# Optimization experiments

Hardware: AMD Instinct MI355X
Metric: run time of the kernel (lower is better)

## Reference

```python
import jax, jax.numpy as jnp
import numpy as np

B, S, C, P, M, H = 64, 512, 862, 96, 512, 128  # batch, seq_len, enc_in, pred_len, mem_num, hid_size


def setup_inputs() -> dict:
    key = jax.random.key(0)
    ks = jax.random.split(key, 8)
    x = jax.random.normal(ks[0], (B, S, C), dtype=jnp.float32)
    # nn.Linear default init scale ~ 1/sqrt(fan_in)
    W1 = jax.random.normal(ks[1], (H, S), dtype=jnp.float32) / np.float32(np.sqrt(S))
    b1 = jnp.zeros((H,), dtype=jnp.float32)
    Wp = jax.random.normal(ks[2], (H, H), dtype=jnp.float32) / np.float32(np.sqrt(H))
    bp = jnp.zeros((H,), dtype=jnp.float32)
    W2 = jax.random.normal(ks[3], (P, 2 * H), dtype=jnp.float32) / np.float32(np.sqrt(2 * H))
    b2 = jnp.zeros((P,), dtype=jnp.float32)
    # xavier_normal_ with relu gain: std = sqrt(2) * sqrt(2/(fan_in+fan_out))
    mem_std = np.float32(np.sqrt(2.0) * np.sqrt(2.0 / (M + H)))
    memory = jax.random.normal(ks[4], (M, H), dtype=jnp.float32) * mem_std
    return dict(x=x, W1=W1, b1=b1, Wp=Wp, bp=bp, W2=W2, b2=b2, memory=memory)


def reference(x, W1, b1, Wp, bp, W2, b2, memory):
    b, s, c = x.shape
    # get_repre: Linear1 over seq dim, sigmoid, projector
    r = jax.nn.sigmoid(jnp.einsum('bsc,hs->bch', x, W1) + b1)   # [B, C, H]
    r = jnp.einsum('bch,gh->bcg', r, Wp) + bp                    # [B, C, H]
    r = r.reshape(-1, H)                                         # [N, H], N = B*C
    # memory_enhance: codebook attention (topk/distance loss does not affect output)
    att = jax.nn.softmax(jnp.einsum('nd,fd->nf', r, memory), axis=1)  # [N, M]
    out = jnp.einsum('nf,fd->nd', att, memory)                        # [N, H]
    rep = jnp.concatenate([out, r], axis=1).reshape(b, c, 2 * H)      # [B, C, 2H]
    # predict: Linear2 then permute to [B, pred_len, C]
    res = jnp.einsum('bcd,pd->bcp', rep, W2) + b2
    return jnp.transpose(res, (0, 2, 1))
```

## Files before the change

kernel.cpp:

```cpp
#include <hip/hip_runtime.h>
#include <hip/hip_bf16.h>

typedef __attribute__((ext_vector_type(4))) float f32x4;
typedef __attribute__((ext_vector_type(8))) short s16x8;

#define DEVI __device__ __forceinline__

constexpr int S = 512, C = 862, P = 96, H = 128, BATCH = 64;

DEVI short f2bf(float f) {
  unsigned u = __builtin_bit_cast(unsigned, f);
  u += 0x7fffu + ((u >> 16) & 1u);
  return (short)(u >> 16);
}

DEVI unsigned pk2(float a, float b) {
  return (unsigned)(unsigned short)f2bf(a) | ((unsigned)(unsigned short)f2bf(b) << 16);
}

DEVI s16x8 mk8(const float* v) {
  s16x8 r;
#pragma unroll
  for (int i = 0; i < 8; ++i) r[i] = f2bf(v[i]);
  return r;
}

DEVI void gload16(const void* g, void* l) {
  __builtin_amdgcn_global_load_lds(
      (const __attribute__((address_space(1))) void*)g,
      (__attribute__((address_space(3))) void*)l, 16, 0, 0);
}

template <int NK>
DEVI void redistN(const unsigned* p01, const unsigned* p23, int sA, int hi,
                  s16x8* f) {
#pragma unroll
  for (int kc = 0; kc < NK; ++kc) {
    unsigned a0 = __shfl(p01[2 * kc], sA),      b0 = __shfl(p01[2 * kc + 1], sA);
    unsigned a1 = __shfl(p23[2 * kc], sA),      b1 = __shfl(p23[2 * kc + 1], sA);
    unsigned a2 = __shfl(p01[2 * kc], sA + 16), b2 = __shfl(p01[2 * kc + 1], sA + 16);
    unsigned a3 = __shfl(p23[2 * kc], sA + 16), b3 = __shfl(p23[2 * kc + 1], sA + 16);
    union { s16x8 v; unsigned u[4]; } t;
    t.u[0] = hi ? b0 : a0;
    t.u[1] = hi ? b1 : a1;
    t.u[2] = hi ? b2 : a2;
    t.u[3] = hi ? b3 : a3;
    f[kc] = t.v;
  }
}

__global__ __launch_bounds__(256) void k0_convert(
    const float* __restrict__ W1, const float* __restrict__ Wp,
    const float* __restrict__ W2, const float* __restrict__ mem,
    short* __restrict__ W1b, short* __restrict__ WpS, short* __restrict__ W2b,
    short* __restrict__ membS, short* __restrict__ memTS) {
  int i = blockIdx.x * 256 + threadIdx.x;
  if (i < 65536) { W1b[i] = f2bf(W1[i]); return; }
  i -= 65536;
  if (i < 16384) {
    int g = i >> 7, h = i & 127;
    WpS[(g << 7) + (h ^ ((g & 7) << 3))] = f2bf(Wp[i]);
    return;
  }
  i -= 16384;
  if (i < 24576) { W2b[i] = f2bf(W2[i]); return; }
  i -= 24576;
  if (i < 65536) {
    int f = i >> 7, d = i & 127;
    short v = f2bf(mem[i]);
    membS[((f >> 6) << 13) + ((f & 63) << 7) + (d ^ ((f & 7) << 3))] = v;
    memTS[((f >> 6) << 13) + (d << 6) + ((f & 63) ^ ((d & 7) << 3))] = v;
  }
}

__global__ __launch_bounds__(512, 2) void k12_fused(
    const float* __restrict__ x, const short* __restrict__ W1b,
    const float* __restrict__ b1, const short* __restrict__ WpS,
    const float* __restrict__ bp, const short* __restrict__ membS,
    const short* __restrict__ memTS, const short* __restrict__ W2b,
    const float* __restrict__ b2, float* __restrict__ out) {
  __shared__ __align__(16) char lds[65536];
  short* xt0 = (short*)(lds);
  short* xt1 = (short*)(lds + 16384);
  short* w1t0 = (short*)(lds + 32768);
  short* w1t1 = (short*)(lds + 49152);
  float* resf = (float*)lds;

  const int b = blockIdx.y, c0 = blockIdx.x * 128;
  const int valid = (C - c0 < 128) ? (C - c0) : 128;
  const int tid = threadIdx.x, l = tid & 63, w = tid >> 6;
  const int l15 = l & 15, l4 = l >> 4;
  const int sA = l15 + 32 * (l4 & 1);
  const int hi = (l4 >> 1) & 1;
  const int xr = (l15 & 7) << 4;
  const int cb = l4 * 16;
  const int rloc = 16 * w + l15;

  s16x8 rb[4];
  {
    const int cme = tid & 127, o2 = tid >> 7;
    const bool cv = (c0 + cme) < C;
    const float* xsrc0 = x + (size_t)b * S * C + c0 + cme;
    const int hh = tid >> 2, qq = tid & 3;

    f32x4 acc[8];
#pragma unroll
    for (int t = 0; t < 8; ++t) acc[t] = (f32x4){0.f, 0.f, 0.f, 0.f};

    float xv[2][8];
    s16x8 wv[2];
    {
#pragma unroll
      for (int j = 0; j < 2; ++j) {
        const float* src = xsrc0 + (size_t)((o2 + j * 4) * 8) * C;
#pragma unroll
        for (int i = 0; i < 8; ++i) xv[j][i] = cv ? src[(size_t)i * C] : 0.f;
      }
      const short* wsrc = W1b + hh * 512;
      wv[0] = *(const s16x8*)&wsrc[qq * 8];
      wv[1] = *(const s16x8*)&wsrc[(qq + 4) * 8];
    }

    for (int kt = 0; kt < 8; ++kt) {
      short* xt = (kt & 1) ? xt1 : xt0;
      short* w1t = (kt & 1) ? w1t1 : w1t0;
#pragma unroll
      for (int j = 0; j < 2; ++j)
        *(s16x8*)&xt[cme * 64 + ((o2 + j * 4) ^ (cme & 7)) * 8] = mk8(xv[j]);
      *(s16x8*)&w1t[hh * 64 + (qq ^ (hh & 7)) * 8] = wv[0];
      *(s16x8*)&w1t[hh * 64 + ((qq + 4) ^ (hh & 7)) * 8] = wv[1];
      __syncthreads();
      if (kt < 7) {
        int kn = kt + 1;
#pragma unroll
        for (int j = 0; j < 2; ++j) {
          const float* src = xsrc0 + (size_t)(kn * 64 + (o2 + j * 4) * 8) * C;
#pragma unroll
          for (int i = 0; i < 8; ++i) xv[j][i] = cv ? src[(size_t)i * C] : 0.f;
        }
        const short* wsrc = W1b + hh * 512 + kn * 64;
        wv[0] = *(const s16x8*)&wsrc[qq * 8];
        wv[1] = *(const s16x8*)&wsrc[(qq + 4) * 8];
      }
      s16x8 bx[2];
#pragma unroll
      for (int kc = 0; kc < 2; ++kc)
        bx[kc] = *(const s16x8*)&xt[rloc * 64 + ((kc * 4 + l4) ^ (l15 & 7)) * 8];
#pragma unroll
      for (int t = 0; t < 8; ++t) {
#pragma unroll
        for (int kc = 0; kc < 2; ++kc) {
          s16x8 af = *(const s16x8*)&w1t[(t * 16 + l15) * 64 + ((kc * 4 + l4) ^ (l15 & 7)) * 8];
          acc[t] = __builtin_amdgcn_mfma_f32_16x16x32_bf16(af, bx[kc], acc[t], 0, 0, 0);
        }
      }
      if (kt == 7) __syncthreads();
    }

    unsigned p01[8], p23[8];
#pragma unroll
    for (int t = 0; t < 8; ++t) {
      f32x4 bq = *(const f32x4*)&b1[t * 16 + l4 * 4];
      float s0 = 1.f / (1.f + __expf(-(acc[t][0] + bq[0])));
      float s1 = 1.f / (1.f + __expf(-(acc[t][1] + bq[1])));
      float s2 = 1.f / (1.f + __expf(-(acc[t][2] + bq[2])));
      float s3 = 1.f / (1.f + __expf(-(acc[t][3] + bq[3])));
      p01[t] = pk2(s0, s1);
      p23[t] = pk2(s2, s3);
    }
    redistN<4>(p01, p23, sA, hi, rb);
  }

  {
    const char* gwp = (const char*)WpS;
    const char* gmb = (const char*)membS;
    const char* gmt = (const char*)memTS;
#pragma unroll
    for (int i = 0; i < 4; ++i) {
      int o = (w * 4 + i) * 1024;
      gload16(gwp + o + l * 16, lds + 32768 + o);
    }
#pragma unroll
    for (int i = 0; i < 2; ++i) {
      int o = (w * 2 + i) * 1024;
      gload16(gmb + o + l * 16, lds + o);
      gload16(gmt + o + l * 16, lds + 16384 + o);
    }
  }
  __syncthreads();

  unsigned rpk01[8], rpk23[8];
  {
    const char* bufWp = lds + 32768;
#pragma unroll
    for (int gt = 0; gt < 8; ++gt) {
      f32x4 acc = (f32x4){0.f, 0.f, 0.f, 0.f};
#pragma unroll
      for (int kc = 0; kc < 4; ++kc) {
        s16x8 af = *(const s16x8*)(bufWp + (gt * 16 + l15) * 256 + ((kc * 64 + cb) ^ xr));
        acc = __builtin_amdgcn_mfma_f32_16x16x32_bf16(af, rb[kc], acc, 0, 0, 0);
      }
      f32x4 bq = *(const f32x4*)&bp[gt * 16 + l4 * 4];
      rpk01[gt] = pk2(acc[0] + bq[0], acc[1] + bq[1]);
      rpk23[gt] = pk2(acc[2] + bq[2], acc[3] + bq[3]);
    }
  }
  s16x8 r2f[4];
  redistN<4>(rpk01, rpk23, sA, hi, r2f);
  __syncthreads();

  float m_run = -1e30f, s_run = 0.f;
  f32x4 oacc[8];
#pragma unroll
  for (int dt = 0; dt < 8; ++dt) oacc[dt] = (f32x4){0.f, 0.f, 0.f, 0.f};

  for (int s = 0; s < 8; ++s) {
    char* bufp = lds + ((s & 1) << 15);
    if (s < 7) {
      char* bufn = lds + (((s + 1) & 1) << 15);
      const char* gmb = (const char*)membS + (size_t)(s + 1) * 16384;
      const char* gmt = (const char*)memTS + (size_t)(s + 1) * 16384;
#pragma unroll
      for (int i = 0; i < 2; ++i) {
        int o = (w * 2 + i) * 1024;
        gload16(gmb + o + l * 16, bufn + o);
        gload16(gmt + o + l * 16, bufn + 16384 + o);
      }
    }
    f32x4 lg[4];
#pragma unroll
    for (int ft = 0; ft < 4; ++ft) {
      lg[ft] = (f32x4){0.f, 0.f, 0.f, 0.f};
#pragma unroll
      for (int kc = 0; kc < 4; ++kc) {
        s16x8 af = *(const s16x8*)(bufp + (ft * 16 + l15) * 256 + ((kc * 64 + cb) ^ xr));
        lg[ft] = __builtin_amdgcn_mfma_f32_16x16x32_bf16(af, r2f[kc], lg[ft], 0, 0, 0);
      }
    }
    float mx = lg[0][0];
#pragma unroll
    for (int ft = 0; ft < 4; ++ft)
#pragma unroll
      for (int e = 0; e < 4; ++e) mx = fmaxf(mx, lg[ft][e]);
    mx = fmaxf(mx, __shfl_xor(mx, 16));
    mx = fmaxf(mx, __shfl_xor(mx, 32));
    float mn = fmaxf(m_run, mx);
    float sc = __expf(m_run - mn);
    float ps = 0.f;
#pragma unroll
    for (int ft = 0; ft < 4; ++ft)
#pragma unroll
      for (int e = 0; e < 4; ++e) {
        float p = __expf(lg[ft][e] - mn);
        lg[ft][e] = p;
        ps += p;
      }
    ps += __shfl_xor(ps, 16);
    ps += __shfl_xor(ps, 32);
    s_run = s_run * sc + ps;
    m_run = mn;
#pragma unroll
    for (int dt = 0; dt < 8; ++dt)
#pragma unroll
      for (int e = 0; e < 4; ++e) oacc[dt][e] *= sc;
    unsigned ppk01[4], ppk23[4];
#pragma unroll
    for (int ft = 0; ft < 4; ++ft) {
      ppk01[ft] = pk2(lg[ft][0], lg[ft][1]);
      ppk23[ft] = pk2(lg[ft][2], lg[ft][3]);
    }
    s16x8 pf[2];
    redistN<2>(ppk01, ppk23, sA, hi, pf);
#pragma unroll
    for (int dt = 0; dt < 8; ++dt) {
#pragma unroll
      for (int kc = 0; kc < 2; ++kc) {
        s16x8 af = *(const s16x8*)(bufp + 16384 + (dt * 16 + l15) * 128 + ((kc * 64 + cb) ^ xr));
        oacc[dt] = __builtin_amdgcn_mfma_f32_16x16x32_bf16(af, pf[kc], oacc[dt], 0, 0, 0);
      }
    }
    __syncthreads();
  }

  s16x8 of[4];
  {
    float inv = 1.f / s_run;
    unsigned opk01[8], opk23[8];
#pragma unroll
    for (int dt = 0; dt < 8; ++dt) {
      opk01[dt] = pk2(oacc[dt][0] * inv, oacc[dt][1] * inv);
      opk23[dt] = pk2(oacc[dt][2] * inv, oacc[dt][3] * inv);
    }
    redistN<4>(opk01, opk23, sA, hi, of);
  }

#pragma unroll
  for (int pt = 0; pt < 6; ++pt) {
    f32x4 acc = (f32x4){0.f, 0.f, 0.f, 0.f};
#pragma unroll
    for (int kc = 0; kc < 4; ++kc) {
      s16x8 af = *(const s16x8*)&W2b[(pt * 16 + l15) * 256 + kc * 32 + l4 * 8];
      acc = __builtin_amdgcn_mfma_f32_16x16x32_bf16(af, of[kc], acc, 0, 0, 0);
    }
#pragma unroll
    for (int kc = 0; kc < 4; ++kc) {
      s16x8 af = *(const s16x8*)&W2b[(pt * 16 + l15) * 256 + 128 + kc * 32 + l4 * 8];
      acc = __builtin_amdgcn_mfma_f32_16x16x32_bf16(af, r2f[kc], acc, 0, 0, 0);
    }
    f32x4 bq = *(const f32x4*)&b2[pt * 16 + l4 * 4];
#pragma unroll
    for (int e = 0; e < 4; ++e)
      resf[rloc * 97 + pt * 16 + l4 * 4 + e] = acc[e] + bq[e];
  }
  __syncthreads();
  {
    int c = tid & 127, p0 = tid >> 7;
    if (c < valid) {
      float* dst = out + (size_t)b * P * C + c0 + c;
#pragma unroll
      for (int j = 0; j < 24; ++j) {
        int p = p0 + j * 4;
        dst[(size_t)p * C] = resf[c * 97 + p];
      }
    }
  }
}

extern "C" void kernel_launch(void* const* d_in, const int* in_sizes, int n_in,
                              void* d_out, int out_size, void* d_ws, size_t ws_size,
                              hipStream_t stream) {
  const float* x   = (const float*)d_in[0];
  const float* W1  = (const float*)d_in[1];
  const float* b1  = (const float*)d_in[2];
  const float* Wp  = (const float*)d_in[3];
  const float* bpv = (const float*)d_in[4];
  const float* W2  = (const float*)d_in[5];
  const float* b2  = (const float*)d_in[6];
  const float* mem = (const float*)d_in[7];
  char* ws = (char*)d_ws;
  short* W1b   = (short*)(ws);
  short* WpS   = (short*)(ws + 131072);
  short* W2b   = (short*)(ws + 163840);
  short* membS = (short*)(ws + 212992);
  short* memTS = (short*)(ws + 344064);
  float* outp = (float*)d_out;

  k0_convert<<<672, 256, 0, stream>>>(W1, Wp, W2, mem, W1b, WpS, W2b, membS, memTS);
  dim3 grid(7, BATCH);
  k12_fused<<<grid, 512, 0, stream>>>(x, W1b, b1, WpS, bpv, membS, memTS, W2b, b2, outp);
}
```

Measured before the change: 83.85 us.

## Software-pipeline codebook attention loop and skip online-softmax rescale when max is stable

Restructures the memory-attention loop so the score MFMAs for chunk i+1 run alongside the value MFMAs for chunk i, with separate double buffers for the memory and transposed-memory tiles. It also adds a lazy-rescale test that skips rescaling the running max and accumulator unless the new max exceeds the old by more than 8, and raises launch bounds from 2 to 4 blocks per SM. This aims to hide softmax latency and LDS load stalls and to cut ALU work. The risks are extra register pressure from the 4-block bound, which may cause spills, and a loss of precision if probabilities grow as large as e^8.

```diff
diff --git a/kernel.cpp b/kernel.cpp
--- a/kernel.cpp
+++ b/kernel.cpp
@@ -73,7 +73,7 @@
   }
 }
 
-__global__ __launch_bounds__(512, 2) void k12_fused(
+__global__ __launch_bounds__(512, 4) void k12_fused(
     const float* __restrict__ x, const short* __restrict__ W1b,
     const float* __restrict__ b1, const short* __restrict__ WpS,
     const float* __restrict__ bp, const short* __restrict__ membS,
@@ -174,7 +174,6 @@
   {
     const char* gwp = (const char*)WpS;
     const char* gmb = (const char*)membS;
-    const char* gmt = (const char*)memTS;
 #pragma unroll
     for (int i = 0; i < 4; ++i) {
       int o = (w * 4 + i) * 1024;
@@ -184,7 +183,6 @@
     for (int i = 0; i < 2; ++i) {
       int o = (w * 2 + i) * 1024;
       gload16(gmb + o + l * 16, lds + o);
-      gload16(gmt + o + l * 16, lds + 16384 + o);
     }
   }
   __syncthreads();
@@ -207,33 +205,21 @@
   }
   s16x8 r2f[4];
   redistN<4>(rpk01, rpk23, sA, hi, r2f);
-  __syncthreads();
-
-  float m_run = -1e30f, s_run = 0.f;
+
+  float m_run, s_run;
   f32x4 oacc[8];
 #pragma unroll
   for (int dt = 0; dt < 8; ++dt) oacc[dt] = (f32x4){0.f, 0.f, 0.f, 0.f};
-
-  for (int s = 0; s < 8; ++s) {
-    char* bufp = lds + ((s & 1) << 15);
-    if (s < 7) {
-      char* bufn = lds + (((s + 1) & 1) << 15);
-      const char* gmb = (const char*)membS + (size_t)(s + 1) * 16384;
-      const char* gmt = (const char*)memTS + (size_t)(s + 1) * 16384;
-#pragma unroll
-      for (int i = 0; i < 2; ++i) {
-        int o = (w * 2 + i) * 1024;
-        gload16(gmb + o + l * 16, bufn + o);
-        gload16(gmt + o + l * 16, bufn + 16384 + o);
-      }
-    }
+  s16x8 pfb[2][2];
+
+  {
     f32x4 lg[4];
 #pragma unroll
     for (int ft = 0; ft < 4; ++ft) {
       lg[ft] = (f32x4){0.f, 0.f, 0.f, 0.f};
 #pragma unroll
       for (int kc = 0; kc < 4; ++kc) {
-        s16x8 af = *(const s16x8*)(bufp + (ft * 16 + l15) * 256 + ((kc * 64 + cb) ^ xr));
+        s16x8 af = *(const s16x8*)(lds + (ft * 16 + l15) * 256 + ((kc * 64 + cb) ^ xr));
         lg[ft] = __builtin_amdgcn_mfma_f32_16x16x32_bf16(af, r2f[kc], lg[ft], 0, 0, 0);
       }
     }
@@ -244,43 +230,130 @@
       for (int e = 0; e < 4; ++e) mx = fmaxf(mx, lg[ft][e]);
     mx = fmaxf(mx, __shfl_xor(mx, 16));
     mx = fmaxf(mx, __shfl_xor(mx, 32));
-    float mn = fmaxf(m_run, mx);
-    float sc = __expf(m_run - mn);
+    m_run = mx;
     float ps = 0.f;
-#pragma unroll
-    for (int ft = 0; ft < 4; ++ft)
+    unsigned ppk01[4], ppk23[4];
+#pragma unroll
+    for (int ft = 0; ft < 4; ++ft) {
 #pragma unroll
       for (int e = 0; e < 4; ++e) {
-        float p = __expf(lg[ft][e] - mn);
+        float p = __expf(lg[ft][e] - m_run);
         lg[ft][e] = p;
         ps += p;
       }
+      ppk01[ft] = pk2(lg[ft][0], lg[ft][1]);
+      ppk23[ft] = pk2(lg[ft][2], lg[ft][3]);
+    }
     ps += __shfl_xor(ps, 16);
     ps += __shfl_xor(ps, 32);
-    s_run = s_run * sc + ps;
-    m_run = mn;
-#pragma unroll
-    for (int dt = 0; dt < 8; ++dt)
-#pragma unroll
-      for (int e = 0; e < 4; ++e) oacc[dt][e] *= sc;
-    unsigned ppk01[4], ppk23[4];
-#pragma unroll
-    for (int ft = 0; ft < 4; ++ft) {
-      ppk01[ft] = pk2(lg[ft][0], lg[ft][1]);
-      ppk23[ft] = pk2(lg[ft][2], lg[ft][3]);
-    }
-    s16x8 pf[2];
-    redistN<2>(ppk01, ppk23, sA, hi, pf);
+    s_run = ps;
+    redistN<2>(ppk01, ppk23, sA, hi, pfb[0]);
+  }
+  __syncthreads();
+  {
+    const char* gmb = (const char*)membS + 16384;
+    const char* gmt = (const char*)memTS;
+#pragma unroll
+    for (int i = 0; i < 2; ++i) {
+      int o = (w * 2 + i) * 1024;
+      gload16(gmb + o + l * 16, lds + 16384 + o);
+      gload16(gmt + o + l * 16, lds + 32768 + o);
+    }
+  }
+
+#pragma unroll
+  for (int i = 0; i < 7; ++i) {
+    __syncthreads();
+    if (i < 6) {
+      const char* gmb = (const char*)membS + (size_t)(i + 2) * 16384;
+#pragma unroll
+      for (int j2 = 0; j2 < 2; ++j2) {
+        int o = (w * 2 + j2) * 1024;
+        gload16(gmb + o + l * 16, lds + ((i & 1) << 14) + o);
+      }
+    }
+    {
+      const char* gmt = (const char*)memTS + (size_t)(i + 1) * 16384;
+#pragma unroll
+      for (int j2 = 0; j2 < 2; ++j2) {
+        int o = (w * 2 + j2) * 1024;
+        gload16(gmt + o + l * 16, lds + 32768 + (((i + 1) & 1) << 14) + o);
+      }
+    }
+    f32x4 lg[4];
+    {
+      const char* bmb = lds + (((i + 1) & 1) << 14);
+#pragma unroll
+      for (int ft = 0; ft < 4; ++ft) {
+        lg[ft] = (f32x4){0.f, 0.f, 0.f, 0.f};
+#pragma unroll
+        for (int kc = 0; kc < 4; ++kc) {
+          s16x8 af = *(const s16x8*)(bmb + (ft * 16 + l15) * 256 + ((kc * 64 + cb) ^ xr));
+          lg[ft] = __builtin_amdgcn_mfma_f32_16x16x32_bf16(af, r2f[kc], lg[ft], 0, 0, 0);
+        }
+      }
+    }
+    {
+      const char* bmt = lds + 32768 + ((i & 1) << 14);
+#pragma unroll
+      for (int dt = 0; dt < 8; ++dt) {
+#pragma unroll
+        for (int kc = 0; kc < 2; ++kc) {
+          s16x8 af = *(const s16x8*)(bmt + (dt * 16 + l15) * 128 + ((kc * 64 + cb) ^ xr));
+          oacc[dt] = __builtin_amdgcn_mfma_f32_16x16x32_bf16(af, pfb[i & 1][kc], oacc[dt], 0, 0, 0);
+        }
+      }
+    }
+    {
+      float mx = lg[0][0];
+#pragma unroll
+      for (int ft = 0; ft < 4; ++ft)
+#pragma unroll
+        for (int e = 0; e < 4; ++e) mx = fmaxf(mx, lg[ft][e]);
+      mx = fmaxf(mx, __shfl_xor(mx, 16));
+      mx = fmaxf(mx, __shfl_xor(mx, 32));
+      if (!__all(mx <= m_run + 8.f)) {
+        float mn = fmaxf(m_run, mx);
+        float sc = __expf(m_run - mn);
+        s_run *= sc;
+        m_run = mn;
+#pragma unroll
+        for (int dt = 0; dt < 8; ++dt)
+#pragma unroll
+          for (int e = 0; e < 4; ++e) oacc[dt][e] *= sc;
+      }
+      float ps = 0.f;
+      unsigned ppk01[4], ppk23[4];
+#pragma unroll
+      for (int ft = 0; ft < 4; ++ft) {
+#pragma unroll
+        for (int e = 0; e < 4; ++e) {
+          float p = __expf(lg[ft][e] - m_run);
+          lg[ft][e] = p;
+          ps += p;
+        }
+        ppk01[ft] = pk2(lg[ft][0], lg[ft][1]);
+        ppk23[ft] = pk2(lg[ft][2], lg[ft][3]);
+      }
+      ps += __shfl_xor(ps, 16);
+      ps += __shfl_xor(ps, 32);
+      s_run += ps;
+      redistN<2>(ppk01, ppk23, sA, hi, pfb[(i + 1) & 1]);
+    }
+  }
+  __syncthreads();
+  {
+    const char* bmt = lds + 32768 + 16384;
 #pragma unroll
     for (int dt = 0; dt < 8; ++dt) {
 #pragma unroll
       for (int kc = 0; kc < 2; ++kc) {
-        s16x8 af = *(const s16x8*)(bufp + 16384 + (dt * 16 + l15) * 128 + ((kc * 64 + cb) ^ xr));
-        oacc[dt] = __builtin_amdgcn_mfma_f32_16x16x32_bf16(af, pf[kc], oacc[dt], 0, 0, 0);
-      }
-    }
-    __syncthreads();
-  }
+        s16x8 af = *(const s16x8*)(bmt + (dt * 16 + l15) * 128 + ((kc * 64 + cb) ^ xr));
+        oacc[dt] = __builtin_amdgcn_mfma_f32_16x16x32_bf16(af, pfb[1][kc], oacc[dt], 0, 0, 0);
+      }
+    }
+  }
+  __syncthreads();
 
   s16x8 of[4];
   {
```

Result: no change. 83.41 us (-0.5%).

## Shrink LDS footprint, restage memory buffers, and skip softmax rescale when max stable

Applied to the files above, without the earlier changes.

Cuts shared memory from 64KB to about 48.5KB by single-buffering the W1/x tiles and loading the transposed memory tile each step without prefetch. Only the memory (logit) tile stays double-buffered. Launch bounds are raised from 2 to 6 blocks per CU to allow more concurrent blocks. The online softmax now skips rescaling the accumulators unless the new max exceeds the running max by more than 8, which saves exp and multiply work. The costs are more barriers per step and a non-prefetched transposed-memory load, and the lazy rescale allows exponentials up to e^8 before rescaling.

```diff
diff --git a/kernel.cpp b/kernel.cpp
--- a/kernel.cpp
+++ b/kernel.cpp
@@ -73,17 +73,13 @@
   }
 }
 
-__global__ __launch_bounds__(512, 2) void k12_fused(
+__global__ __launch_bounds__(512, 6) void k12_fused(
     const float* __restrict__ x, const short* __restrict__ W1b,
     const float* __restrict__ b1, const short* __restrict__ WpS,
     const float* __restrict__ bp, const short* __restrict__ membS,
     const short* __restrict__ memTS, const short* __restrict__ W2b,
     const float* __restrict__ b2, float* __restrict__ out) {
-  __shared__ __align__(16) char lds[65536];
-  short* xt0 = (short*)(lds);
-  short* xt1 = (short*)(lds + 16384);
-  short* w1t0 = (short*)(lds + 32768);
-  short* w1t1 = (short*)(lds + 49152);
+  __shared__ __align__(16) char lds[49664];
   float* resf = (float*)lds;
 
   const int b = blockIdx.y, c0 = blockIdx.x * 128;
@@ -98,6 +94,8 @@
 
   s16x8 rb[4];
   {
+    short* xt = (short*)lds;
+    short* w1t = (short*)(lds + 16384);
     const int cme = tid & 127, o2 = tid >> 7;
     const bool cv = (c0 + cme) < C;
     const float* xsrc0 = x + (size_t)b * S * C + c0 + cme;
@@ -122,8 +120,6 @@
     }
 
     for (int kt = 0; kt < 8; ++kt) {
-      short* xt = (kt & 1) ? xt1 : xt0;
-      short* w1t = (kt & 1) ? w1t1 : w1t0;
 #pragma unroll
       for (int j = 0; j < 2; ++j)
         *(s16x8*)&xt[cme * 64 + ((o2 + j * 4) ^ (cme & 7)) * 8] = mk8(xv[j]);
@@ -154,7 +150,22 @@
           acc[t] = __builtin_amdgcn_mfma_f32_16x16x32_bf16(af, bx[kc], acc[t], 0, 0, 0);
         }
       }
-      if (kt == 7) __syncthreads();
+      __syncthreads();
+    }
+
+    {
+      const char* gwp = (const char*)WpS;
+      const char* gmb = (const char*)membS;
+#pragma unroll
+      for (int i = 0; i < 4; ++i) {
+        int o = (w * 4 + i) * 1024;
+        gload16(gwp + o + l * 16, lds + 16384 + o);
+      }
+#pragma unroll
+      for (int i = 0; i < 2; ++i) {
+        int o = (w * 2 + i) * 1024;
+        gload16(gmb + o + l * 16, lds + o);
+      }
     }
 
     unsigned p01[8], p23[8];
@@ -170,28 +181,11 @@
     }
     redistN<4>(p01, p23, sA, hi, rb);
   }
-
-  {
-    const char* gwp = (const char*)WpS;
-    const char* gmb = (const char*)membS;
-    const char* gmt = (const char*)memTS;
-#pragma unroll
-    for (int i = 0; i < 4; ++i) {
-      int o = (w * 4 + i) * 1024;
-      gload16(gwp + o + l * 16, lds + 32768 + o);
-    }
-#pragma unroll
-    for (int i = 0; i < 2; ++i) {
-      int o = (w * 2 + i) * 1024;
-      gload16(gmb + o + l * 16, lds + o);
-      gload16(gmt + o + l * 16, lds + 16384 + o);
-    }
-  }
   __syncthreads();
 
   unsigned rpk01[8], rpk23[8];
   {
-    const char* bufWp = lds + 32768;
+    const char* bufWp = lds + 16384;
 #pragma unroll
     for (int gt = 0; gt < 8; ++gt) {
       f32x4 acc = (f32x4){0.f, 0.f, 0.f, 0.f};
@@ -207,80 +201,96 @@
   }
   s16x8 r2f[4];
   redistN<4>(rpk01, rpk23, sA, hi, r2f);
-  __syncthreads();
 
   float m_run = -1e30f, s_run = 0.f;
   f32x4 oacc[8];
 #pragma unroll
   for (int dt = 0; dt < 8; ++dt) oacc[dt] = (f32x4){0.f, 0.f, 0.f, 0.f};
 
-  for (int s = 0; s < 8; ++s) {
-    char* bufp = lds + ((s & 1) << 15);
-    if (s < 7) {
-      char* bufn = lds + (((s + 1) & 1) << 15);
-      const char* gmb = (const char*)membS + (size_t)(s + 1) * 16384;
-      const char* gmt = (const char*)memTS + (size_t)(s + 1) * 16384;
+  for (int s5 = 0; s5 < 8; ++s5) {
+    __syncthreads();
+    {
+      const char* gmt = (const char*)memTS + (size_t)s5 * 16384;
 #pragma unroll
       for (int i = 0; i < 2; ++i) {
         int o = (w * 2 + i) * 1024;
-        gload16(gmb + o + l * 16, bufn + o);
-        gload16(gmt + o + l * 16, bufn + 16384 + o);
+        gload16(gmt + o + l * 16, lds + 32768 + o);
+      }
+    }
+    if (s5 < 7) {
+      const char* gmb = (const char*)membS + (size_t)(s5 + 1) * 16384;
+#pragma unroll
+      for (int i = 0; i < 2; ++i) {
+        int o = (w * 2 + i) * 1024;
+        gload16(gmb + o + l * 16, lds + (((s5 + 1) & 1) << 14) + o);
       }
     }
     f32x4 lg[4];
-#pragma unroll
-    for (int ft = 0; ft < 4; ++ft) {
-      lg[ft] = (f32x4){0.f, 0.f, 0.f, 0.f};
-#pragma unroll
-      for (int kc = 0; kc < 4; ++kc) {
-        s16x8 af = *(const s16x8*)(bufp + (ft * 16 + l15) * 256 + ((kc * 64 + cb) ^ xr));
-        lg[ft] = __builtin_amdgcn_mfma_f32_16x16x32_bf16(af, r2f[kc], lg[ft], 0, 0, 0);
-      }
-    }
-    float mx = lg[0][0];
-#pragma unroll
-    for (int ft = 0; ft < 4; ++ft)
-#pragma unroll
-      for (int e = 0; e < 4; ++e) mx = fmaxf(mx, lg[ft][e]);
-    mx = fmaxf(mx, __shfl_xor(mx, 16));
-    mx = fmaxf(mx, __shfl_xor(mx, 32));
-    float mn = fmaxf(m_run, mx);
-    float sc = __expf(m_run - mn);
-    float ps = 0.f;
-#pragma unroll
-    for (int ft = 0; ft < 4; ++ft)
-#pragma unroll
-      for (int e = 0; e < 4; ++e) {
-        float p = __expf(lg[ft][e] - mn);
-        lg[ft][e] = p;
-        ps += p;
-      }
-    ps += __shfl_xor(ps, 16);
-    ps += __shfl_xor(ps, 32);
-    s_run = s_run * sc + ps;
-    m_run = mn;
-#pragma unroll
-    for (int dt = 0; dt < 8; ++dt)
-#pragma unroll
-      for (int e = 0; e < 4; ++e) oacc[dt][e] *= sc;
-    unsigned ppk01[4], ppk23[4];
-#pragma unroll
-    for (int ft = 0; ft < 4; ++ft) {
-      ppk01[ft] = pk2(lg[ft][0], lg[ft][1]);
-      ppk23[ft] = pk2(lg[ft][2], lg[ft][3]);
+    {
+      const char* bmb = lds + ((s5 & 1) << 14);
+#pragma unroll
+      for (int ft = 0; ft < 4; ++ft) {
+        lg[ft] = (f32x4){0.f, 0.f, 0.f, 0.f};
+#pragma unroll
+        for (int kc = 0; kc < 4; ++kc) {
+          s16x8 af = *(const s16x8*)(bmb + (ft * 16 + l15) * 256 + ((kc * 64 + cb) ^ xr));
+          lg[ft] = __builtin_amdgcn_mfma_f32_16x16x32_bf16(af, r2f[kc], lg[ft], 0, 0, 0);
+        }
+      }
     }
     s16x8 pf[2];
-    redistN<2>(ppk01, ppk23, sA, hi, pf);
-#pragma unroll
-    for (int dt = 0; dt < 8; ++dt) {
-#pragma unroll
-      for (int kc = 0; kc < 2; ++kc) {
-        s16x8 af = *(const s16x8*)(bufp + 16384 + (dt * 16 + l15) * 128 + ((kc * 64 + cb) ^ xr));
-        oacc[dt] = __builtin_amdgcn_mfma_f32_16x16x32_bf16(af, pf[kc], oacc[dt], 0, 0, 0);
-      }
+    {
+      float mx = lg[0][0];
+#pragma unroll
+      for (int ft = 0; ft < 4; ++ft)
+#pragma unroll
+        for (int e = 0; e < 4; ++e) mx = fmaxf(mx, lg[ft][e]);
+      mx = fmaxf(mx, __shfl_xor(mx, 16));
+      mx = fmaxf(mx, __shfl_xor(mx, 32));
+      if (s5 == 0) {
+        m_run = mx;
+      } else if (!__all(mx <= m_run + 8.f)) {
+        float mn = fmaxf(m_run, mx);
+        float sc = __expf(m_run - mn);
+        s_run *= sc;
+        m_run = mn;
+#pragma unroll
+        for (int dt = 0; dt < 8; ++dt)
+#pragma unroll
+          for (int e = 0; e < 4; ++e) oacc[dt][e] *= sc;
+      }
+      float ps = 0.f;
+      unsigned ppk01[4], ppk23[4];
+#pragma unroll
+      for (int ft = 0; ft < 4; ++ft) {
+#pragma unroll
+        for (int e = 0; e < 4; ++e) {
+          float p = __expf(lg[ft][e] - m_run);
+          lg[ft][e] = p;
+          ps += p;
+        }
+        ppk01[ft] = pk2(lg[ft][0], lg[ft][1]);
+        ppk23[ft] = pk2(lg[ft][2], lg[ft][3]);
+      }
+      ps += __shfl_xor(ps, 16);
+      ps += __shfl_xor(ps, 32);
+      s_run += ps;
+      redistN<2>(ppk01, ppk23, sA, hi, pf);
     }
     __syncthreads();
-  }
+    {
+      const char* bmt = lds + 32768;
+#pragma unroll
+      for (int dt = 0; dt < 8; ++dt) {
+#pragma unroll
+        for (int kc = 0; kc < 2; ++kc) {
+          s16x8 af = *(const s16x8*)(bmt + (dt * 16 + l15) * 128 + ((kc * 64 + cb) ^ xr));
+          oacc[dt] = __builtin_amdgcn_mfma_f32_16x16x32_bf16(af, pf[kc], oacc[dt], 0, 0, 0);
+        }
+      }
+    }
+  }
+  __syncthreads();
 
   s16x8 of[4];
   {
```

New measurement: 104.0 us. +24.0%, slower.
